# Performance work log

Hardware: AMD Instinct MI355X
Metric: run time of the kernel (lower is better)

## Reference

```python
import jax, jax.numpy as jnp
import numpy as np
import math

N_NODES = 100000
N_EDGES = 1600000
D_FEAT = 32
K = 1        # Bernstein index k
N_ORD = 2    # Bernstein order n
COMB = float(math.comb(N_ORD, K))


def setup_inputs() -> dict:
    key = jax.random.key(0)
    k1, k2, k3 = jax.random.split(key, 3)
    feat = jax.random.normal(k1, (N_NODES, D_FEAT), dtype=jnp.float32)
    edge_src = jax.random.randint(k2, (N_EDGES,), 0, N_NODES)
    edge_dst = jax.random.randint(k3, (N_EDGES,), 0, N_NODES)
    return {"feat": feat, "edge_src": edge_src, "edge_dst": edge_dst}


def reference(feat, edge_src, edge_dst):
    # in-degree of each node (copy_u/sum aggregates over incoming edges)
    deg = jax.ops.segment_sum(jnp.ones((N_EDGES,), feat.dtype), edge_dst,
                              num_segments=N_NODES)
    d_invsqrt = jnp.clip(deg, 1.0, None) ** -0.5  # [N]
    d_invsqrt = d_invsqrt[:, None]                 # [N,1]

    def unn_laplacian(x):
        msg = (x * d_invsqrt)[edge_src]            # [E,D]
        agg = jax.ops.segment_sum(msg, edge_dst, num_segments=N_NODES)
        return x - agg * d_invsqrt

    if K == 0:
        h = feat
        for _ in range(N_ORD):
            h = unn_laplacian(h) / 2
            h = feat - h
    elif K == N_ORD:
        h = feat
        for _ in range(N_ORD):
            h = unn_laplacian(h) / 2
    else:
        temp = feat
        for _ in range(K):
            temp = unn_laplacian(temp) / 2
        h = feat
        for _ in range(N_ORD - K):
            h = unn_laplacian(h) / 2
            h = feat - h
        h = temp * h
    return COMB * h
```

## Files before the change

### kernel.cpp

```cpp
#include <hip/hip_runtime.h>

#define N_NODES 100000
#define N_EDGES 1600000
#define D_FEAT 32

#define BSH 7
#define BMASK 127
#define NB 782
#define CAPB 2432

#define P1_BS 512
#define P1_TILE 4096
#define P1_CAP 16


static __device__ __forceinline__ unsigned pack_bf16(float a, float b) {
    unsigned ua = __float_as_uint(a);
    unsigned ub = __float_as_uint(b);
    ua = (ua + 0x7FFFu + ((ua >> 16) & 1u)) >> 16;
    ub = (ub + 0x7FFFu + ((ub >> 16) & 1u)) >> 16;
    return (ua & 0xFFFFu) | (ub << 16);
}

__global__ void __launch_bounds__(P1_BS)
bucket_kernel(const int* __restrict__ edge_src,
              const int* __restrict__ edge_dst,
              int* __restrict__ cursorA,
              int* __restrict__ pairs, int n_edges) {
    __shared__ int s_cnt[NB];
    __shared__ int s_base[NB];
    __shared__ int s_off[NB + 1];
    __shared__ int s_buf[NB * P1_CAP];

    int tile = blockIdx.x * P1_TILE;
    if (tile >= n_edges) return;

    for (int b = threadIdx.x; b < NB; b += P1_BS) s_cnt[b] = 0;
    __syncthreads();

    const int4* src4 = reinterpret_cast<const int4*>(edge_src);
    const int4* dst4 = reinterpret_cast<const int4*>(edge_dst);
    int tileq = blockIdx.x * (P1_TILE / 4);
    #pragma unroll
    for (int j = 0; j < P1_TILE / 4 / P1_BS; ++j) {
        int iq = tileq + j * P1_BS + threadIdx.x;
        if (iq * 4 < n_edges) {
            int4 sv = src4[iq];
            int4 dv = dst4[iq];
            int ss[4] = {sv.x, sv.y, sv.z, sv.w};
            int dd[4] = {dv.x, dv.y, dv.z, dv.w};
            #pragma unroll
            for (int u = 0; u < 4; ++u) {
                int b = dd[u] >> BSH;
                int packed = (ss[u] << BSH) | (dd[u] & BMASK);
                int p = atomicAdd(&s_cnt[b], 1);
                if (p < P1_CAP) {
                    s_buf[b * P1_CAP + p] = packed;
                } else {
                    int gp = atomicAdd(&cursorA[b], 1);
                    if (gp < CAPB) pairs[b * CAPB + gp] = packed;
                }
            }
        }
    }
    __syncthreads();

    for (int b = threadIdx.x; b < NB; b += P1_BS) {
        int c = min(s_cnt[b], P1_CAP);
        s_base[b] = b * CAPB + atomicAdd(&cursorA[b], c);
        s_cnt[b] = c;
    }
    __syncthreads();
    if (threadIdx.x == 0) {
        int acc = 0;
        for (int b = 0; b < NB; ++b) { s_off[b] = acc; acc += s_cnt[b]; }
        s_off[NB] = acc;
    }
    __syncthreads();

    int total = s_off[NB];
    for (int t = threadIdx.x; t < total; t += P1_BS) {
        int lo = 0, hi = NB;
        while (hi - lo > 1) {
            int mid = (lo + hi) >> 1;
            if (t >= s_off[mid]) lo = mid; else hi = mid;
        }
        int idx = t - s_off[lo];
        pairs[s_base[lo] + idx] = s_buf[lo * P1_CAP + idx];
    }
}

__global__ void __launch_bounds__(256)
hist_kernel(const int* __restrict__ pairs,
            const int* __restrict__ cursorA,
            const float* __restrict__ feat,
            float* __restrict__ dinv,
            unsigned* __restrict__ sfeat) {
    __shared__ int h[128];
    __shared__ float dv_s[128];
    int b = blockIdx.x;
    int t = threadIdx.x;
    int base = b * CAPB;
    int cnt = min(cursorA[b], CAPB);

    if (t < 128) h[t] = 0;
    __syncthreads();
    for (int i = t; i < cnt; i += 256)
        atomicAdd(&h[pairs[base + i] & BMASK], 1);
    __syncthreads();
    if (t < 128) {
        float dvv = rsqrtf(fmaxf((float)h[t], 1.0f));
        dv_s[t] = dvv;
        int node = (b << BSH) + t;
        if (node < N_NODES) dinv[node] = dvv;
    }
    __syncthreads();

    const float4* feat4 = reinterpret_cast<const float4*>(feat);
    uint4* sf4 = reinterpret_cast<uint4*>(sfeat);
    for (int idx = t; idx < 128 * 4; idx += 256) {
        int nl = idx >> 2;
        int q = idx & 3;
        int node = (b << BSH) + nl;
        if (node >= N_NODES) continue;
        float dvv = dv_s[nl];
        float4 fa = feat4[node * 8 + 2 * q];
        float4 fb = feat4[node * 8 + 2 * q + 1];
        uint4 pk;
        pk.x = pack_bf16(fa.x * dvv, fa.y * dvv);
        pk.y = pack_bf16(fa.z * dvv, fa.w * dvv);
        pk.z = pack_bf16(fb.x * dvv, fb.y * dvv);
        pk.w = pack_bf16(fb.z * dvv, fb.w * dvv);
        sf4[node * 4 + q] = pk;
    }
}

__global__ void __launch_bounds__(256)
sortgather_kernel(const int* __restrict__ pairs,
                  const int* __restrict__ cursorA,
                  const float* __restrict__ feat,
                  const unsigned* __restrict__ sfeat,
                  float* __restrict__ out) {
    __shared__ int buf[CAPB];
    __shared__ int outb[CAPB];
    __shared__ int h[128];
    __shared__ int sc[128];
    __shared__ int cur[128];
    __shared__ int exs[128];
    __shared__ int cnl[128];
    __shared__ float dv_s[128];

    int b = blockIdx.x;
    int t = threadIdx.x;
    int base = b * CAPB;
    int cnt = min(cursorA[b], CAPB);

    if (t < 128) h[t] = 0;
    __syncthreads();
    for (int i = t; i < cnt; i += 256) {
        int p = pairs[base + i];
        buf[i] = p;
        atomicAdd(&h[p & BMASK], 1);
    }
    __syncthreads();

    int v = 0;
    if (t < 128) { v = h[t]; sc[t] = v; }
    __syncthreads();
    for (int off = 1; off < 128; off <<= 1) {
        int x = 0;
        if (t < 128 && t >= off) x = sc[t - off];
        __syncthreads();
        if (t < 128) sc[t] += x;
        __syncthreads();
    }
    if (t < 128) {
        int ex = sc[t] - v;
        cur[t] = ex;
        exs[t] = ex;
        cnl[t] = v;
        dv_s[t] = rsqrtf(fmaxf((float)v, 1.0f));
    }
    __syncthreads();

    for (int i = t; i < cnt; i += 256) {
        int p = buf[i];
        int pos = atomicAdd(&cur[p & BMASK], 1);
        outb[pos] = p >> BSH;
    }
    __syncthreads();

    const uint4* sf4 = reinterpret_cast<const uint4*>(sfeat);
    const float4* feat4 = reinterpret_cast<const float4*>(feat);
    float4* out4 = reinterpret_cast<float4*>(out);

    #define ACC(r)                                                 \
        a0 += __uint_as_float((r).x << 16);                        \
        a1 += __uint_as_float((r).x & 0xFFFF0000u);                \
        a2 += __uint_as_float((r).y << 16);                        \
        a3 += __uint_as_float((r).y & 0xFFFF0000u);                \
        a4 += __uint_as_float((r).z << 16);                        \
        a5 += __uint_as_float((r).z & 0xFFFF0000u);                \
        a6 += __uint_as_float((r).w << 16);                        \
        a7 += __uint_as_float((r).w & 0xFFFF0000u);

    #pragma unroll
    for (int pass = 0; pass < 2; ++pass) {
        int item = t + pass * 256;
        int nl = item >> 2;
        int q = item & 3;
        int node = (b << BSH) + nl;
        if (node >= N_NODES) continue;
        int k = exs[nl];
        int en = k + cnl[nl];
        float a0 = 0.f, a1 = 0.f, a2 = 0.f, a3 = 0.f;
        float a4 = 0.f, a5 = 0.f, a6 = 0.f, a7 = 0.f;
        for (; k + 3 < en; k += 4) {
            int s0 = outb[k],     s1 = outb[k + 1];
            int s2 = outb[k + 2], s3 = outb[k + 3];
            uint4 r0 = sf4[s0 * 4 + q];
            uint4 r1 = sf4[s1 * 4 + q];
            uint4 r2 = sf4[s2 * 4 + q];
            uint4 r3 = sf4[s3 * 4 + q];
            ACC(r0) ACC(r1) ACC(r2) ACC(r3)
        }
        for (; k < en; ++k) {
            uint4 r = sf4[outb[k] * 4 + q];
            ACC(r)
        }
        float dvn = dv_s[nl];
        float4 fa = feat4[node * 8 + 2 * q];
        float4 fb = feat4[node * 8 + 2 * q + 1];
        float4 oa, ob;
        float y;
        y = 0.5f * (fa.x - a0 * dvn); oa.x = 2.0f * y * (fa.x - y);
        y = 0.5f * (fa.y - a1 * dvn); oa.y = 2.0f * y * (fa.y - y);
        y = 0.5f * (fa.z - a2 * dvn); oa.z = 2.0f * y * (fa.z - y);
        y = 0.5f * (fa.w - a3 * dvn); oa.w = 2.0f * y * (fa.w - y);
        y = 0.5f * (fb.x - a4 * dvn); ob.x = 2.0f * y * (fb.x - y);
        y = 0.5f * (fb.y - a5 * dvn); ob.y = 2.0f * y * (fb.y - y);
        y = 0.5f * (fb.z - a6 * dvn); ob.z = 2.0f * y * (fb.z - y);
        y = 0.5f * (fb.w - a7 * dvn); ob.w = 2.0f * y * (fb.w - y);
        out4[node * 8 + 2 * q] = oa;
        out4[node * 8 + 2 * q + 1] = ob;
    }
    #undef ACC
}

extern "C" void kernel_launch(void* const* d_in, const int* in_sizes, int n_in,
                              void* d_out, int out_size, void* d_ws, size_t ws_size,
                              hipStream_t stream) {
    const float* feat = (const float*)d_in[0];
    const int* edge_src = (const int*)d_in[1];
    const int* edge_dst = (const int*)d_in[2];
    float* out = (float*)d_out;

    int* ws = (int*)d_ws;
    int* cursorA    = ws;
    float* dinv     = (float*)(cursorA + 1024);
    int* pairs      = (int*)(dinv + N_NODES);
    unsigned* sfeat = (unsigned*)(pairs + NB * CAPB);

    hipMemsetAsync(cursorA, 0, 1024 * sizeof(int), stream);
    {
        int blocks = (N_EDGES + P1_TILE - 1) / P1_TILE;
        bucket_kernel<<<blocks, P1_BS, 0, stream>>>(edge_src, edge_dst,
                                                    cursorA, pairs, N_EDGES);
    }
    hist_kernel<<<NB, 256, 0, stream>>>(pairs, cursorA, feat, dinv, sfeat);
    sortgather_kernel<<<NB, 256, 0, stream>>>(pairs, cursorA, feat, sfeat, out);
}
```

Before: 133.4 us.

## Compute in-degree with global atomics in bucket pass, drop per-bucket histogram kernel

The bucketing kernel now also counts each node's in-degree with a global atomic per edge into a zeroed array. That lets the separate histogram kernel, which re-read all bucketed pairs, be replaced by a flat elementwise kernel that scales and packs the features. The sort-gather kernel reads the degrees directly, skipping its own shared histogram pass, and runs 512 threads per block so each thread handles one node-quarter in a single pass. The trade-off is 1.6M scattered global atomics plus a larger memset, in exchange for one less full read of the pairs array and fewer shared atomics.

New measurement: 184.8 us. 38.6% more time.

```diff
diff --git a/kernel.cpp b/kernel.cpp
--- a/kernel.cpp
+++ b/kernel.cpp
@@ -26,6 +26,7 @@
 bucket_kernel(const int* __restrict__ edge_src,
               const int* __restrict__ edge_dst,
               int* __restrict__ cursorA,
+              int* __restrict__ cnt_g,
               int* __restrict__ pairs, int n_edges) {
     __shared__ int s_cnt[NB];
     __shared__ int s_base[NB];
@@ -51,6 +52,7 @@
             int dd[4] = {dv.x, dv.y, dv.z, dv.w};
             #pragma unroll
             for (int u = 0; u < 4; ++u) {
+                atomicAdd(&cnt_g[dd[u]], 1);
                 int b = dd[u] >> BSH;
                 int packed = (ss[u] << BSH) | (dd[u] & BMASK);
                 int p = atomicAdd(&s_cnt[b], 1);
@@ -90,60 +92,35 @@
     }
 }
 
-__global__ void __launch_bounds__(256)
-hist_kernel(const int* __restrict__ pairs,
-            const int* __restrict__ cursorA,
-            const float* __restrict__ feat,
-            float* __restrict__ dinv,
-            unsigned* __restrict__ sfeat) {
-    __shared__ int h[128];
-    __shared__ float dv_s[128];
-    int b = blockIdx.x;
-    int t = threadIdx.x;
-    int base = b * CAPB;
-    int cnt = min(cursorA[b], CAPB);
-
-    if (t < 128) h[t] = 0;
-    __syncthreads();
-    for (int i = t; i < cnt; i += 256)
-        atomicAdd(&h[pairs[base + i] & BMASK], 1);
-    __syncthreads();
-    if (t < 128) {
-        float dvv = rsqrtf(fmaxf((float)h[t], 1.0f));
-        dv_s[t] = dvv;
-        int node = (b << BSH) + t;
-        if (node < N_NODES) dinv[node] = dvv;
-    }
-    __syncthreads();
-
+__global__ void sf_kernel(const float* __restrict__ feat,
+                          const int* __restrict__ cnt_g,
+                          unsigned* __restrict__ sfeat) {
+    int gid = blockIdx.x * blockDim.x + threadIdx.x;
+    int total = N_NODES * 4;
+    if (gid >= total) return;
+    int node = gid >> 2;
+    int q = gid & 3;
+    float dvv = rsqrtf(fmaxf((float)cnt_g[node], 1.0f));
     const float4* feat4 = reinterpret_cast<const float4*>(feat);
-    uint4* sf4 = reinterpret_cast<uint4*>(sfeat);
-    for (int idx = t; idx < 128 * 4; idx += 256) {
-        int nl = idx >> 2;
-        int q = idx & 3;
-        int node = (b << BSH) + nl;
-        if (node >= N_NODES) continue;
-        float dvv = dv_s[nl];
-        float4 fa = feat4[node * 8 + 2 * q];
-        float4 fb = feat4[node * 8 + 2 * q + 1];
-        uint4 pk;
-        pk.x = pack_bf16(fa.x * dvv, fa.y * dvv);
-        pk.y = pack_bf16(fa.z * dvv, fa.w * dvv);
-        pk.z = pack_bf16(fb.x * dvv, fb.y * dvv);
-        pk.w = pack_bf16(fb.z * dvv, fb.w * dvv);
-        sf4[node * 4 + q] = pk;
-    }
-}
-
-__global__ void __launch_bounds__(256)
+    float4 fa = feat4[node * 8 + 2 * q];
+    float4 fb = feat4[node * 8 + 2 * q + 1];
+    uint4 pk;
+    pk.x = pack_bf16(fa.x * dvv, fa.y * dvv);
+    pk.y = pack_bf16(fa.z * dvv, fa.w * dvv);
+    pk.z = pack_bf16(fb.x * dvv, fb.y * dvv);
+    pk.w = pack_bf16(fb.z * dvv, fb.w * dvv);
+    reinterpret_cast<uint4*>(sfeat)[node * 4 + q] = pk;
+}
+
+__global__ void __launch_bounds__(512)
 sortgather_kernel(const int* __restrict__ pairs,
                   const int* __restrict__ cursorA,
+                  const int* __restrict__ cnt_g,
                   const float* __restrict__ feat,
                   const unsigned* __restrict__ sfeat,
                   float* __restrict__ out) {
     __shared__ int buf[CAPB];
     __shared__ int outb[CAPB];
-    __shared__ int h[128];
     __shared__ int sc[128];
     __shared__ int cur[128];
     __shared__ int exs[128];
@@ -155,17 +132,14 @@
     int base = b * CAPB;
     int cnt = min(cursorA[b], CAPB);
 
-    if (t < 128) h[t] = 0;
-    __syncthreads();
-    for (int i = t; i < cnt; i += 256) {
-        int p = pairs[base + i];
-        buf[i] = p;
-        atomicAdd(&h[p & BMASK], 1);
-    }
-    __syncthreads();
-
+    for (int i = t; i < cnt; i += 512)
+        buf[i] = pairs[base + i];
     int v = 0;
-    if (t < 128) { v = h[t]; sc[t] = v; }
+    if (t < 128) {
+        int node = (b << BSH) + t;
+        v = (node < N_NODES) ? cnt_g[node] : 0;
+        sc[t] = v;
+    }
     __syncthreads();
     for (int off = 1; off < 128; off <<= 1) {
         int x = 0;
@@ -183,7 +157,7 @@
     }
     __syncthreads();
 
-    for (int i = t; i < cnt; i += 256) {
+    for (int i = t; i < cnt; i += 512) {
         int p = buf[i];
         int pos = atomicAdd(&cur[p & BMASK], 1);
         outb[pos] = p >> BSH;
@@ -204,47 +178,44 @@
         a6 += __uint_as_float((r).w << 16);                        \
         a7 += __uint_as_float((r).w & 0xFFFF0000u);
 
-    #pragma unroll
-    for (int pass = 0; pass < 2; ++pass) {
-        int item = t + pass * 256;
-        int nl = item >> 2;
-        int q = item & 3;
-        int node = (b << BSH) + nl;
-        if (node >= N_NODES) continue;
-        int k = exs[nl];
-        int en = k + cnl[nl];
-        float a0 = 0.f, a1 = 0.f, a2 = 0.f, a3 = 0.f;
-        float a4 = 0.f, a5 = 0.f, a6 = 0.f, a7 = 0.f;
-        for (; k + 3 < en; k += 4) {
-            int s0 = outb[k],     s1 = outb[k + 1];
-            int s2 = outb[k + 2], s3 = outb[k + 3];
-            uint4 r0 = sf4[s0 * 4 + q];
-            uint4 r1 = sf4[s1 * 4 + q];
-            uint4 r2 = sf4[s2 * 4 + q];
-            uint4 r3 = sf4[s3 * 4 + q];
-            ACC(r0) ACC(r1) ACC(r2) ACC(r3)
-        }
-        for (; k < en; ++k) {
-            uint4 r = sf4[outb[k] * 4 + q];
-            ACC(r)
-        }
-        float dvn = dv_s[nl];
-        float4 fa = feat4[node * 8 + 2 * q];
-        float4 fb = feat4[node * 8 + 2 * q + 1];
-        float4 oa, ob;
-        float y;
-        y = 0.5f * (fa.x - a0 * dvn); oa.x = 2.0f * y * (fa.x - y);
-        y = 0.5f * (fa.y - a1 * dvn); oa.y = 2.0f * y * (fa.y - y);
-        y = 0.5f * (fa.z - a2 * dvn); oa.z = 2.0f * y * (fa.z - y);
-        y = 0.5f * (fa.w - a3 * dvn); oa.w = 2.0f * y * (fa.w - y);
-        y = 0.5f * (fb.x - a4 * dvn); ob.x = 2.0f * y * (fb.x - y);
-        y = 0.5f * (fb.y - a5 * dvn); ob.y = 2.0f * y * (fb.y - y);
-        y = 0.5f * (fb.z - a6 * dvn); ob.z = 2.0f * y * (fb.z - y);
-        y = 0.5f * (fb.w - a7 * dvn); ob.w = 2.0f * y * (fb.w - y);
-        out4[node * 8 + 2 * q] = oa;
-        out4[node * 8 + 2 * q + 1] = ob;
+    int nl = t >> 2;
+    int q = t & 3;
+    int node = (b << BSH) + nl;
+    if (node >= N_NODES) return;
+    int k = exs[nl];
+    int en = k + cnl[nl];
+    float a0 = 0.f, a1 = 0.f, a2 = 0.f, a3 = 0.f;
+    float a4 = 0.f, a5 = 0.f, a6 = 0.f, a7 = 0.f;
+    for (; k + 3 < en; k += 4) {
+        int s0 = outb[k],     s1 = outb[k + 1];
+        int s2 = outb[k + 2], s3 = outb[k + 3];
+        uint4 r0 = sf4[s0 * 4 + q];
+        uint4 r1 = sf4[s1 * 4 + q];
+        uint4 r2 = sf4[s2 * 4 + q];
+        uint4 r3 = sf4[s3 * 4 + q];
+        ACC(r0) ACC(r1) ACC(r2) ACC(r3)
+    }
+    for (; k < en; ++k) {
+        uint4 r = sf4[outb[k] * 4 + q];
+        ACC(r)
     }
     #undef ACC
+
+    float dvn = dv_s[nl];
+    float4 fa = feat4[node * 8 + 2 * q];
+    float4 fb = feat4[node * 8 + 2 * q + 1];
+    float4 oa, ob;
+    float y;
+    y = 0.5f * (fa.x - a0 * dvn); oa.x = 2.0f * y * (fa.x - y);
+    y = 0.5f * (fa.y - a1 * dvn); oa.y = 2.0f * y * (fa.y - y);
+    y = 0.5f * (fa.z - a2 * dvn); oa.z = 2.0f * y * (fa.z - y);
+    y = 0.5f * (fa.w - a3 * dvn); oa.w = 2.0f * y * (fa.w - y);
+    y = 0.5f * (fb.x - a4 * dvn); ob.x = 2.0f * y * (fb.x - y);
+    y = 0.5f * (fb.y - a5 * dvn); ob.y = 2.0f * y * (fb.y - y);
+    y = 0.5f * (fb.z - a6 * dvn); ob.z = 2.0f * y * (fb.z - y);
+    y = 0.5f * (fb.w - a7 * dvn); ob.w = 2.0f * y * (fb.w - y);
+    out4[node * 8 + 2 * q] = oa;
+    out4[node * 8 + 2 * q + 1] = ob;
 }
 
 extern "C" void kernel_launch(void* const* d_in, const int* in_sizes, int n_in,
@@ -257,16 +228,22 @@
 
     int* ws = (int*)d_ws;
     int* cursorA    = ws;
-    float* dinv     = (float*)(cursorA + 1024);
-    int* pairs      = (int*)(dinv + N_NODES);
+    int* cnt_g      = cursorA + 1024;
+    int* pairs      = cnt_g + N_NODES;
     unsigned* sfeat = (unsigned*)(pairs + NB * CAPB);
 
-    hipMemsetAsync(cursorA, 0, 1024 * sizeof(int), stream);
+    hipMemsetAsync(cursorA, 0, (size_t)(1024 + N_NODES) * sizeof(int), stream);
     {
         int blocks = (N_EDGES + P1_TILE - 1) / P1_TILE;
         bucket_kernel<<<blocks, P1_BS, 0, stream>>>(edge_src, edge_dst,
-                                                    cursorA, pairs, N_EDGES);
-    }
-    hist_kernel<<<NB, 256, 0, stream>>>(pairs, cursorA, feat, dinv, sfeat);
-    sortgather_kernel<<<NB, 256, 0, stream>>>(pairs, cursorA, feat, sfeat, out);
-}
+                                                    cursorA, cnt_g, pairs,
+                                                    N_EDGES);
+    }
+    {
+        int total = N_NODES * 4;
+        int blocks = (total + 255) / 256;
+        sf_kernel<<<blocks, 256, 0, stream>>>(feat, cnt_g, sfeat);
+    }
+    sortgather_kernel<<<NB, 512, 0, stream>>>(pairs, cursorA, cnt_g, feat,
+                                              sfeat, out);
+}
```

## Replace per-bucket counting sort with shared-memory atomic scatter aggregation

Applied to the files above, without the earlier changes.

The aggregation kernel no longer counting-sorts each bucket's edges by destination. Each edge now gathers its source's bf16 row and atomically adds it into a swizzled 128x32 fp32 accumulator in shared memory, running with 512 threads per block. The bucket kernel uses smaller tiles (2048 edges, 8-entry local cap), which launches more blocks, and the unused dinv output is dropped. This removes the prefix scan and scatter passes at the cost of many LDS float atomics and a nondeterministic summation order.

New measurement: 454.0 us. 3.4x slower.

```diff
diff --git a/kernel.cpp b/kernel.cpp
--- a/kernel.cpp
+++ b/kernel.cpp
@@ -10,8 +10,8 @@
 #define CAPB 2432
 
 #define P1_BS 512
-#define P1_TILE 4096
-#define P1_CAP 16
+#define P1_TILE 2048
+#define P1_CAP 8
 
 
 static __device__ __forceinline__ unsigned pack_bf16(float a, float b) {
@@ -40,26 +40,22 @@
 
     const int4* src4 = reinterpret_cast<const int4*>(edge_src);
     const int4* dst4 = reinterpret_cast<const int4*>(edge_dst);
-    int tileq = blockIdx.x * (P1_TILE / 4);
-    #pragma unroll
-    for (int j = 0; j < P1_TILE / 4 / P1_BS; ++j) {
-        int iq = tileq + j * P1_BS + threadIdx.x;
-        if (iq * 4 < n_edges) {
-            int4 sv = src4[iq];
-            int4 dv = dst4[iq];
-            int ss[4] = {sv.x, sv.y, sv.z, sv.w};
-            int dd[4] = {dv.x, dv.y, dv.z, dv.w};
-            #pragma unroll
-            for (int u = 0; u < 4; ++u) {
-                int b = dd[u] >> BSH;
-                int packed = (ss[u] << BSH) | (dd[u] & BMASK);
-                int p = atomicAdd(&s_cnt[b], 1);
-                if (p < P1_CAP) {
-                    s_buf[b * P1_CAP + p] = packed;
-                } else {
-                    int gp = atomicAdd(&cursorA[b], 1);
-                    if (gp < CAPB) pairs[b * CAPB + gp] = packed;
-                }
+    int iq = blockIdx.x * (P1_TILE / 4) + threadIdx.x;
+    if (iq * 4 < n_edges) {
+        int4 sv = src4[iq];
+        int4 dv = dst4[iq];
+        int ss[4] = {sv.x, sv.y, sv.z, sv.w};
+        int dd[4] = {dv.x, dv.y, dv.z, dv.w};
+        #pragma unroll
+        for (int u = 0; u < 4; ++u) {
+            int b = dd[u] >> BSH;
+            int packed = (ss[u] << BSH) | (dd[u] & BMASK);
+            int p = atomicAdd(&s_cnt[b], 1);
+            if (p < P1_CAP) {
+                s_buf[b * P1_CAP + p] = packed;
+            } else {
+                int gp = atomicAdd(&cursorA[b], 1);
+                if (gp < CAPB) pairs[b * CAPB + gp] = packed;
             }
         }
     }
@@ -91,11 +87,10 @@
 }
 
 __global__ void __launch_bounds__(256)
-hist_kernel(const int* __restrict__ pairs,
-            const int* __restrict__ cursorA,
-            const float* __restrict__ feat,
-            float* __restrict__ dinv,
-            unsigned* __restrict__ sfeat) {
+hist_sf_kernel(const int* __restrict__ pairs,
+               const int* __restrict__ cursorA,
+               const float* __restrict__ feat,
+               unsigned* __restrict__ sfeat) {
     __shared__ int h[128];
     __shared__ float dv_s[128];
     int b = blockIdx.x;
@@ -108,12 +103,7 @@
     for (int i = t; i < cnt; i += 256)
         atomicAdd(&h[pairs[base + i] & BMASK], 1);
     __syncthreads();
-    if (t < 128) {
-        float dvv = rsqrtf(fmaxf((float)h[t], 1.0f));
-        dv_s[t] = dvv;
-        int node = (b << BSH) + t;
-        if (node < N_NODES) dinv[node] = dvv;
-    }
+    if (t < 128) dv_s[t] = rsqrtf(fmaxf((float)h[t], 1.0f));
     __syncthreads();
 
     const float4* feat4 = reinterpret_cast<const float4*>(feat);
@@ -135,19 +125,15 @@
     }
 }
 
-__global__ void __launch_bounds__(256)
-sortgather_kernel(const int* __restrict__ pairs,
-                  const int* __restrict__ cursorA,
-                  const float* __restrict__ feat,
-                  const unsigned* __restrict__ sfeat,
-                  float* __restrict__ out) {
-    __shared__ int buf[CAPB];
-    __shared__ int outb[CAPB];
+__global__ void __launch_bounds__(512)
+agg_kernel(const int* __restrict__ pairs,
+           const int* __restrict__ cursorA,
+           const float* __restrict__ feat,
+           const unsigned* __restrict__ sfeat,
+           float* __restrict__ out) {
+    __shared__ int pairs_s[CAPB];
+    __shared__ float agg_s[128 * 32];
     __shared__ int h[128];
-    __shared__ int sc[128];
-    __shared__ int cur[128];
-    __shared__ int exs[128];
-    __shared__ int cnl[128];
     __shared__ float dv_s[128];
 
     int b = blockIdx.x;
@@ -156,95 +142,68 @@
     int cnt = min(cursorA[b], CAPB);
 
     if (t < 128) h[t] = 0;
-    __syncthreads();
-    for (int i = t; i < cnt; i += 256) {
+    for (int i = t; i < 128 * 32; i += 512) agg_s[i] = 0.0f;
+    __syncthreads();
+    for (int i = t; i < cnt; i += 512) {
         int p = pairs[base + i];
-        buf[i] = p;
+        pairs_s[i] = p;
         atomicAdd(&h[p & BMASK], 1);
     }
     __syncthreads();
-
-    int v = 0;
-    if (t < 128) { v = h[t]; sc[t] = v; }
-    __syncthreads();
-    for (int off = 1; off < 128; off <<= 1) {
-        int x = 0;
-        if (t < 128 && t >= off) x = sc[t - off];
-        __syncthreads();
-        if (t < 128) sc[t] += x;
-        __syncthreads();
-    }
-    if (t < 128) {
-        int ex = sc[t] - v;
-        cur[t] = ex;
-        exs[t] = ex;
-        cnl[t] = v;
-        dv_s[t] = rsqrtf(fmaxf((float)v, 1.0f));
-    }
-    __syncthreads();
-
-    for (int i = t; i < cnt; i += 256) {
-        int p = buf[i];
-        int pos = atomicAdd(&cur[p & BMASK], 1);
-        outb[pos] = p >> BSH;
-    }
+    if (t < 128) dv_s[t] = rsqrtf(fmaxf((float)h[t], 1.0f));
     __syncthreads();
 
     const uint4* sf4 = reinterpret_cast<const uint4*>(sfeat);
+    int q = t & 3;
+    int fb8 = q * 8;
+    for (int e = (t >> 2); e < cnt; e += 128) {
+        int p = pairs_s[e];
+        int dst = p & BMASK;
+        int src = p >> BSH;
+        uint4 r = sf4[src * 4 + q];
+        int rb = dst << 5;
+        int sw = dst & 31;
+        atomicAdd(&agg_s[rb + ((fb8 + 0) ^ sw)], __uint_as_float(r.x << 16));
+        atomicAdd(&agg_s[rb + ((fb8 + 1) ^ sw)], __uint_as_float(r.x & 0xFFFF0000u));
+        atomicAdd(&agg_s[rb + ((fb8 + 2) ^ sw)], __uint_as_float(r.y << 16));
+        atomicAdd(&agg_s[rb + ((fb8 + 3) ^ sw)], __uint_as_float(r.y & 0xFFFF0000u));
+        atomicAdd(&agg_s[rb + ((fb8 + 4) ^ sw)], __uint_as_float(r.z << 16));
+        atomicAdd(&agg_s[rb + ((fb8 + 5) ^ sw)], __uint_as_float(r.z & 0xFFFF0000u));
+        atomicAdd(&agg_s[rb + ((fb8 + 6) ^ sw)], __uint_as_float(r.w << 16));
+        atomicAdd(&agg_s[rb + ((fb8 + 7) ^ sw)], __uint_as_float(r.w & 0xFFFF0000u));
+    }
+    __syncthreads();
+
+    int nl = t >> 2;
+    int node = (b << BSH) + nl;
+    if (node >= N_NODES) return;
+    float dvn = dv_s[nl];
+    int rb = nl << 5;
+    int sw = nl & 31;
+    float a0 = agg_s[rb + ((fb8 + 0) ^ sw)];
+    float a1 = agg_s[rb + ((fb8 + 1) ^ sw)];
+    float a2 = agg_s[rb + ((fb8 + 2) ^ sw)];
+    float a3 = agg_s[rb + ((fb8 + 3) ^ sw)];
+    float a4 = agg_s[rb + ((fb8 + 4) ^ sw)];
+    float a5 = agg_s[rb + ((fb8 + 5) ^ sw)];
+    float a6 = agg_s[rb + ((fb8 + 6) ^ sw)];
+    float a7 = agg_s[rb + ((fb8 + 7) ^ sw)];
     const float4* feat4 = reinterpret_cast<const float4*>(feat);
+    float4 fa = feat4[node * 8 + 2 * q];
+    float4 fbv = feat4[node * 8 + 2 * q + 1];
+    float4 oa, ob;
+    float y;
+    y = 0.5f * (fa.x - a0 * dvn);  oa.x = 2.0f * y * (fa.x - y);
+    y = 0.5f * (fa.y - a1 * dvn);  oa.y = 2.0f * y * (fa.y - y);
+    y = 0.5f * (fa.z - a2 * dvn);  oa.z = 2.0f * y * (fa.z - y);
+    y = 0.5f * (fa.w - a3 * dvn);  oa.w = 2.0f * y * (fa.w - y);
+    y = 0.5f * (fbv.x - a4 * dvn); ob.x = 2.0f * y * (fbv.x - y);
+    y = 0.5f * (fbv.y - a5 * dvn); ob.y = 2.0f * y * (fbv.y - y);
+    y = 0.5f * (fbv.z - a6 * dvn); ob.z = 2.0f * y * (fbv.z - y);
+    y = 0.5f * (fbv.w - a7 * dvn); ob.w = 2.0f * y * (fbv.w - y);
     float4* out4 = reinterpret_cast<float4*>(out);
-
-    #define ACC(r)                                                 \
-        a0 += __uint_as_float((r).x << 16);                        \
-        a1 += __uint_as_float((r).x & 0xFFFF0000u);                \
-        a2 += __uint_as_float((r).y << 16);                        \
-        a3 += __uint_as_float((r).y & 0xFFFF0000u);                \
-        a4 += __uint_as_float((r).z << 16);                        \
-        a5 += __uint_as_float((r).z & 0xFFFF0000u);                \
-        a6 += __uint_as_float((r).w << 16);                        \
-        a7 += __uint_as_float((r).w & 0xFFFF0000u);
-
-    #pragma unroll
-    for (int pass = 0; pass < 2; ++pass) {
-        int item = t + pass * 256;
-        int nl = item >> 2;
-        int q = item & 3;
-        int node = (b << BSH) + nl;
-        if (node >= N_NODES) continue;
-        int k = exs[nl];
-        int en = k + cnl[nl];
-        float a0 = 0.f, a1 = 0.f, a2 = 0.f, a3 = 0.f;
-        float a4 = 0.f, a5 = 0.f, a6 = 0.f, a7 = 0.f;
-        for (; k + 3 < en; k += 4) {
-            int s0 = outb[k],     s1 = outb[k + 1];
-            int s2 = outb[k + 2], s3 = outb[k + 3];
-            uint4 r0 = sf4[s0 * 4 + q];
-            uint4 r1 = sf4[s1 * 4 + q];
-            uint4 r2 = sf4[s2 * 4 + q];
-            uint4 r3 = sf4[s3 * 4 + q];
-            ACC(r0) ACC(r1) ACC(r2) ACC(r3)
-        }
-        for (; k < en; ++k) {
-            uint4 r = sf4[outb[k] * 4 + q];
-            ACC(r)
-        }
-        float dvn = dv_s[nl];
-        float4 fa = feat4[node * 8 + 2 * q];
-        float4 fb = feat4[node * 8 + 2 * q + 1];
-        float4 oa, ob;
-        float y;
-        y = 0.5f * (fa.x - a0 * dvn); oa.x = 2.0f * y * (fa.x - y);
-        y = 0.5f * (fa.y - a1 * dvn); oa.y = 2.0f * y * (fa.y - y);
-        y = 0.5f * (fa.z - a2 * dvn); oa.z = 2.0f * y * (fa.z - y);
-        y = 0.5f * (fa.w - a3 * dvn); oa.w = 2.0f * y * (fa.w - y);
-        y = 0.5f * (fb.x - a4 * dvn); ob.x = 2.0f * y * (fb.x - y);
-        y = 0.5f * (fb.y - a5 * dvn); ob.y = 2.0f * y * (fb.y - y);
-        y = 0.5f * (fb.z - a6 * dvn); ob.z = 2.0f * y * (fb.z - y);
-        y = 0.5f * (fb.w - a7 * dvn); ob.w = 2.0f * y * (fb.w - y);
-        out4[node * 8 + 2 * q] = oa;
-        out4[node * 8 + 2 * q + 1] = ob;
-    }
-    #undef ACC
+    out4[node * 8 + 2 * q] = oa;
+    out4[node * 8 + 2 * q + 1] = ob;
 }
 
 extern "C" void kernel_launch(void* const* d_in, const int* in_sizes, int n_in,
@@ -257,8 +216,7 @@
 
     int* ws = (int*)d_ws;
     int* cursorA    = ws;
-    float* dinv     = (float*)(cursorA + 1024);
-    int* pairs      = (int*)(dinv + N_NODES);
+    int* pairs      = cursorA + 1024;
     unsigned* sfeat = (unsigned*)(pairs + NB * CAPB);
 
     hipMemsetAsync(cursorA, 0, 1024 * sizeof(int), stream);
@@ -267,6 +225,6 @@
         bucket_kernel<<<blocks, P1_BS, 0, stream>>>(edge_src, edge_dst,
                                                     cursorA, pairs, N_EDGES);
     }
-    hist_kernel<<<NB, 256, 0, stream>>>(pairs, cursorA, feat, dinv, sfeat);
-    sortgather_kernel<<<NB, 256, 0, stream>>>(pairs, cursorA, feat, sfeat, out);
-}
+    hist_sf_kernel<<<NB, 256, 0, stream>>>(pairs, cursorA, feat, sfeat);
+    agg_kernel<<<NB, 512, 0, stream>>>(pairs, cursorA, feat, sfeat, out);
+}
```
